# Performance work log

Measured on AMD Instinct MI355X. Metric: run time of the kernel, lower is better.

Reference implementation:

```python
import jax, jax.numpy as jnp
import numpy as np

D = 1024      # embedding_dim
H = 16        # n_heads
HD = D // H   # head_dim = 64
E = 8         # num_experts
K = 2         # top_k
I = 1024      # moe intermediate
S = 2048      # seq_len
B = 1
EPS = 1e-6
THETA = 10000.0


def _rmsnorm(x, w):
    xf = x.astype(jnp.float32)
    var = jnp.mean(xf * xf, axis=-1, keepdims=True)
    return (xf * jax.lax.rsqrt(var + EPS)).astype(x.dtype) * w


def _rope(x, positions):
    # x: [B, S, H, HD], neox-style rotate-half RoPE
    half = HD // 2
    inv_freq = 1.0 / (THETA ** (jnp.arange(0, half, dtype=jnp.float32) / half))
    freqs = positions.astype(jnp.float32)[:, None] * inv_freq[None, :]  # [S, half]
    cos = jnp.cos(freqs)[None, :, None, :]
    sin = jnp.sin(freqs)[None, :, None, :]
    x1, x2 = x[..., :half], x[..., half:]
    return jnp.concatenate([x1 * cos - x2 * sin, x1 * sin + x2 * cos], axis=-1).astype(x.dtype)


def _attn(x, positions, wqkv, wo):
    b, s, _ = x.shape
    qkv = (x @ wqkv).reshape(b, s, 3, H, HD)
    q, k, v = qkv[:, :, 0], qkv[:, :, 1], qkv[:, :, 2]
    q = _rope(q, positions)
    k = _rope(k, positions)
    scale = 1.0 / np.sqrt(HD)
    scores = jnp.einsum('bqhd,bkhd->bhqk', q, k) * scale
    causal = jnp.tril(jnp.ones((s, s), dtype=bool))
    scores = jnp.where(causal[None, None], scores, jnp.finfo(scores.dtype).min)
    probs = jax.nn.softmax(scores, axis=-1)
    o = jnp.einsum('bhqk,bkhd->bqhd', probs, v).reshape(b, s, D)
    return o @ wo


def _moe(x, gate_w, wg, wu, wd):
    # x: [T, D]
    T = x.shape[0]
    logits = x @ gate_w                                    # [T, E]
    probs = jax.nn.softmax(logits.astype(jnp.float32), axis=-1)
    vals, idx = jax.lax.top_k(probs, K)                    # [T, K]
    vals = vals / jnp.sum(vals, axis=-1, keepdims=True)    # renormalize=True
    combine = jnp.zeros((T, E), dtype=jnp.float32)
    combine = combine.at[jnp.arange(T)[:, None], idx].add(vals)
    combine = combine.astype(x.dtype)                      # [T, E]
    out = jnp.zeros_like(x)
    for e in range(E):  # fixed small expert loop; SwiGLU expert FFN
        h = jax.nn.silu(x @ wg[e]) * (x @ wu[e])
        out = out + combine[:, e:e + 1] * (h @ wd[e])
    return out


def setup_inputs() -> dict:
    key = jax.random.key(0)
    ks = jax.random.split(key, 8)
    std = 0.02
    return {
        'positions': jnp.arange(S, dtype=jnp.int32),
        'hidden_states': jax.random.normal(ks[0], (B, S, D), jnp.float32),
        'residual': jax.random.normal(ks[1], (B, S, D), jnp.float32),
        'ln1_w': jnp.ones((D,), jnp.float32),
        'ln2_w': jnp.ones((D,), jnp.float32),
        'wqkv': jax.random.normal(ks[2], (D, 3 * D), jnp.float32) * std,
        'wo': jax.random.normal(ks[3], (D, D), jnp.float32) * std,
        'gate_w': jax.random.normal(ks[4], (D, E), jnp.float32) * std,
        'wg': jax.random.normal(ks[5], (E, D, I), jnp.float32) * std,
        'wu': jax.random.normal(ks[6], (E, D, I), jnp.float32) * std,
        'wd': jax.random.normal(ks[7], (E, I, D), jnp.float32) * std,
    }


def reference(positions, hidden_states, residual, ln1_w, ln2_w, wqkv, wo, gate_w, wg, wu, wd):
    # _forward_with_post_attn_norm: residual arg is overwritten by hidden_states
    res = hidden_states
    x = _rmsnorm(hidden_states, ln1_w)
    x = res + _attn(x, positions, wqkv, wo)
    res2 = x
    y = _rmsnorm(x, ln2_w)
    b, s, _ = y.shape
    moe_out = _moe(y.reshape(-1, D), gate_w, wg, wu, wd).reshape(b, s, D)
    return res2 + moe_out
```

## Files before the change

kernel.cpp:

```cpp
#include <hip/hip_runtime.h>
#include <math.h>

constexpr int S  = 2048;
constexpr int D  = 1024;
constexpr int NH = 16;
constexpr int NE = 8;
constexpr float EPS   = 1e-6f;
constexpr float THETA = 10000.0f;
constexpr float SCL2  = 0.125f * 1.4426950408889634f;
constexpr float LOG2E = 1.4426950408889634f;

typedef unsigned short u16;
typedef unsigned int   u32;
typedef unsigned long long u64;
typedef __attribute__((ext_vector_type(8))) short short8;
typedef __attribute__((ext_vector_type(4))) float f32x4;

__device__ __forceinline__ u16 f2bf(float x) {
  union { float f; u32 u; } v; v.f = x;
  u32 r = (v.u + 0x7FFFu + ((v.u >> 16) & 1u)) >> 16;
  return (u16)r;
}
__device__ __forceinline__ float bf2f(u16 h) {
  union { u32 u; float f; } v; v.u = ((u32)h) << 16;
  return v.f;
}
__device__ __forceinline__ f32x4 mfma16(short8 a, short8 b, f32x4 c) {
  return __builtin_amdgcn_mfma_f32_16x16x32_bf16(a, b, c, 0, 0, 0);
}
__device__ __forceinline__ void gl_lds16(const void* g, void* l) {
  __builtin_amdgcn_global_load_lds((const __attribute__((address_space(1))) u32*)g,
                                   (__attribute__((address_space(3))) u32*)l, 16, 0, 0);
}
__device__ __forceinline__ u64 pack4bf(float a, float b, float c, float d) {
  return (u64)f2bf(a) | ((u64)f2bf(b) << 16) | ((u64)f2bf(c) << 32) | ((u64)f2bf(d) << 48);
}

__global__ __launch_bounds__(256) void prep_kernel(const float* __restrict__ wqkv,
    const float* __restrict__ wo, const float* __restrict__ wg, const float* __restrict__ wu,
    const float* __restrict__ wd, const int* __restrict__ positions,
    const float* __restrict__ hidden, const float* __restrict__ ln1_w,
    u16* __restrict__ wqkvT2, u16* __restrict__ woT2, u16* __restrict__ wgT,
    u16* __restrict__ wuT, u16* __restrict__ wdT, float2* __restrict__ ropetab,
    u16* __restrict__ xn2) {
  const int b = blockIdx.x;
  const int tid = threadIdx.x;
  if (b >= 7424) {
    const int t = b - 7424;
    const float* xr = hidden + (size_t)t * D;
    float v[4]; float ss = 0.f;
#pragma unroll
    for (int i = 0; i < 4; ++i) { v[i] = xr[tid + i * 256]; ss += v[i] * v[i]; }
#pragma unroll
    for (int m = 32; m >= 1; m >>= 1) ss += __shfl_xor(ss, m, 64);
    __shared__ float red[4];
    if ((tid & 63) == 0) red[tid >> 6] = ss;
    __syncthreads();
    const float rs = rsqrtf((red[0] + red[1] + red[2] + red[3]) * (1.f / (float)D) + EPS);
#pragma unroll
    for (int i = 0; i < 4; ++i) {
      const int d = tid + i * 256;
      const float y = v[i] * rs * ln1_w[d];
      const u16 h = f2bf(y);
      xn2[(size_t)t * 2048 + d] = h;
      xn2[(size_t)t * 2048 + 1024 + d] = f2bf(y - bf2f(h));
    }
    return;
  }
  if (b >= 7168) {
    const int idx = (b - 7168) * 256 + tid;
    const int t = idx >> 5, p = idx & 31;
    const float inv = powf(THETA, -(float)p * (1.f / 32.f));
    const float fr = (float)positions[t] * inv;
    float sn, cs; sincosf(fr, &sn, &cs);
    ropetab[idx] = make_float2(cs, sn);
    return;
  }
  __shared__ float t_[64][65];
  const float* W; u16* out; int N, n0, k0; bool split;
  if (b < 768) {
    W = wqkv; out = wqkvT2; N = 3072; split = true;
    n0 = (b % 48) * 64; k0 = (b / 48) * 64;
  } else if (b < 1024) {
    W = wo; out = woT2; N = 1024; split = true;
    const int r = b - 768; n0 = (r & 15) * 64; k0 = (r >> 4) * 64;
  } else {
    int r;
    if (b < 3072)      { r = b - 1024; const int e = r >> 8; W = wg + (size_t)e * 1048576; out = wgT + (size_t)e * 1048576; }
    else if (b < 5120) { r = b - 3072; const int e = r >> 8; W = wu + (size_t)e * 1048576; out = wuT + (size_t)e * 1048576; }
    else               { r = b - 5120; const int e = r >> 8; W = wd + (size_t)e * 1048576; out = wdT + (size_t)e * 1048576; }
    N = 1024; split = false;
    r &= 255; n0 = (r & 15) * 64; k0 = (r >> 4) * 64;
  }
  const int rr = tid >> 4, c4 = (tid & 15) * 4;
#pragma unroll
  for (int i = 0; i < 4; ++i) {
    const float4 v = *(const float4*)(W + (size_t)(k0 + rr + i * 16) * N + n0 + c4);
    t_[rr + i * 16][c4 + 0] = v.x; t_[rr + i * 16][c4 + 1] = v.y;
    t_[rr + i * 16][c4 + 2] = v.z; t_[rr + i * 16][c4 + 3] = v.w;
  }
  __syncthreads();
  if (split) {
#pragma unroll
    for (int i = 0; i < 4; ++i) {
      const int n = n0 + rr + i * 16;
      u16* oh = out + (size_t)n * 2048 + k0 + c4;
      const float v0 = t_[c4 + 0][rr + i * 16], v1 = t_[c4 + 1][rr + i * 16];
      const float v2 = t_[c4 + 2][rr + i * 16], v3 = t_[c4 + 3][rr + i * 16];
      *(u64*)(void*)oh = pack4bf(v0, v1, v2, v3);
      *(u64*)(void*)(oh + 1024) = pack4bf(v0 - bf2f(f2bf(v0)), v1 - bf2f(f2bf(v1)),
                                          v2 - bf2f(f2bf(v2)), v3 - bf2f(f2bf(v3)));
    }
  } else {
#pragma unroll
    for (int i = 0; i < 4; ++i) {
      const int n = n0 + rr + i * 16;
      u16* o = out + (size_t)n * 1024 + k0 + c4;
      *(u64*)(void*)o = pack4bf(t_[c4 + 0][rr + i * 16], t_[c4 + 1][rr + i * 16],
                                t_[c4 + 2][rr + i * 16], t_[c4 + 3][rr + i * 16]);
    }
  }
}

__global__ __launch_bounds__(256) void gemm_qkv(const u16* __restrict__ A2,
    const u16* __restrict__ Bt2, float* __restrict__ Cpart) {
  __shared__ u16 As[2][128 * 32];
  __shared__ u16 Bs[2][128 * 32];
  const int b = blockIdx.x;
  const int xcd = b & 7, ii = b >> 3;
  const int m0 = (ii & 15) * 128;
  const int np = (ii >> 4) % 3, ks = (ii >> 4) / 3;
  const int n0 = (xcd * 3 + np) * 128;
  const int kk0 = ks * 48, kk1 = kk0 + 48;
  const int tid = threadIdx.x, wv = tid >> 6, lane = tid & 63;
  const int l15 = lane & 15, lg = lane >> 4;
  const int wr = wv >> 1, wc = wv & 1;
  const int sr = lane >> 2, sk = (lane & 3) * 16;
  const u16* aptr[2]; const u16* bptr[2];
#pragma unroll
  for (int i = 0; i < 2; ++i) {
    aptr[i] = A2 + (size_t)(m0 + (wv * 2 + i) * 16 + sr) * 2048;
    bptr[i] = Bt2 + (size_t)(n0 + (wv * 2 + i) * 16 + sr) * 2048;
  }
  auto STAGE = [&](int buf, int kk) {
    const int t = kk * 32;
    int ka, kb;
    if (t < 1024)      { ka = t;        kb = t; }
    else if (t < 2048) { ka = t;        kb = t - 1024; }
    else               { ka = t - 2048; kb = t - 1024; }
#pragma unroll
    for (int i = 0; i < 2; ++i) {
      gl_lds16((const char*)(aptr[i] + ka) + sk, (char*)As + buf * 8192 + (wv * 2 + i) * 1024);
      gl_lds16((const char*)(bptr[i] + kb) + sk, (char*)Bs + buf * 8192 + (wv * 2 + i) * 1024);
    }
  };
  f32x4 acc[4][4] = {};
  STAGE(0, kk0);
  __syncthreads();
  int cur = 0;
  for (int kk = kk0; kk < kk1; ++kk) {
    if (kk + 1 < kk1) STAGE(cur ^ 1, kk + 1);
    const u16* Ab = (const u16*)As + cur * 4096;
    const u16* Bb = (const u16*)Bs + cur * 4096;
    short8 a[4], bb[4];
#pragma unroll
    for (int i = 0; i < 4; ++i)
      a[i] = *(const short8*)(const void*)(Ab + (size_t)(wr * 64 + i * 16 + l15) * 32 + lg * 8);
#pragma unroll
    for (int j = 0; j < 4; ++j)
      bb[j] = *(const short8*)(const void*)(Bb + (size_t)(wc * 64 + j * 16 + l15) * 32 + lg * 8);
    __builtin_amdgcn_s_setprio(1);
#pragma unroll
    for (int i = 0; i < 4; ++i)
#pragma unroll
      for (int j = 0; j < 4; ++j) acc[i][j] = mfma16(a[i], bb[j], acc[i][j]);
    __builtin_amdgcn_s_setprio(0);
    __syncthreads();
    cur ^= 1;
  }
  float* P = Cpart + (size_t)ks * S * 3072;
#pragma unroll
  for (int i = 0; i < 4; ++i)
#pragma unroll
    for (int j = 0; j < 4; ++j)
#pragma unroll
      for (int r = 0; r < 4; ++r) {
        const int row = m0 + wr * 64 + i * 16 + lg * 4 + r;
        const int col = n0 + wc * 64 + j * 16 + l15;
        P[(size_t)row * 3072 + col] = acc[i][j][r];
      }
}

__global__ __launch_bounds__(256) void qkv_combine(const float* __restrict__ Cp,
    const float2* __restrict__ tab, u16* __restrict__ Ch, u16* __restrict__ Cl) {
  const int t = blockIdx.x, tid = threadIdx.x;
  const float* r0 = Cp + (size_t)t * 3072;
  const float* r1 = r0 + (size_t)S * 3072;
  const size_t ob = (size_t)t * 3072;
#pragma unroll
  for (int i = 0; i < 4; ++i) {
    const int pi = tid + i * 256;
    const int h = pi >> 5, p = pi & 31;
    const int col = h * 64 + p;
    const float x1 = r0[col] + r1[col];
    const float x2 = r0[col + 32] + r1[col + 32];
    const float2 cs = tab[t * 32 + p];
    const float y1 = x1 * cs.x - x2 * cs.y;
    const float y2 = x1 * cs.y + x2 * cs.x;
    const u16 h1 = f2bf(y1);
    Ch[ob + col] = h1; Cl[ob + col] = f2bf(y1 - bf2f(h1));
    const u16 h2 = f2bf(y2);
    Ch[ob + col + 32] = h2; Cl[ob + col + 32] = f2bf(y2 - bf2f(h2));
  }
#pragma unroll
  for (int i = 0; i < 4; ++i) {
    const int col = 2048 + tid + i * 256;
    const float y = r0[col] + r1[col];
    const u16 h = f2bf(y);
    Ch[ob + col] = h; Cl[ob + col] = f2bf(y - bf2f(h));
  }
}

__global__ __launch_bounds__(256) void gemm_wo(const u16* __restrict__ A2,
    const u16* __restrict__ Bt2, float* __restrict__ Pout) {
  constexpr int N = 1024;
  __shared__ u16 As[2][128 * 32];
  __shared__ u16 Bs[2][128 * 32];
  const int b = blockIdx.x;
  const int xcd = b & 7, ii = b >> 3;
  const int n0 = xcd * 128;
  const int m0 = (ii & 15) * 128;
  const int ks = ii >> 4;
  const int kk0 = ks * 24, kk1 = kk0 + 24;
  const int tid = threadIdx.x, wv = tid >> 6, lane = tid & 63;
  const int l15 = lane & 15, lg = lane >> 4;
  const int wr = wv >> 1, wc = wv & 1;
  const int sr = lane >> 2, sk = (lane & 3) * 16;
  const u16* aptr[2]; const u16* bptr[2];
#pragma unroll
  for (int i = 0; i < 2; ++i) {
    aptr[i] = A2 + (size_t)(m0 + (wv * 2 + i) * 16 + sr) * 2048;
    bptr[i] = Bt2 + (size_t)(n0 + (wv * 2 + i) * 16 + sr) * 2048;
  }
  auto STAGE = [&](int buf, int kk) {
    const int t = kk * 32;
    int ka, kb;
    if (t < 1024)      { ka = t;        kb = t; }
    else if (t < 2048) { ka = t;        kb = t - 1024; }
    else               { ka = t - 2048; kb = t - 1024; }
#pragma unroll
    for (int i = 0; i < 2; ++i) {
      gl_lds16((const char*)(aptr[i] + ka) + sk, (char*)As + buf * 8192 + (wv * 2 + i) * 1024);
      gl_lds16((const char*)(bptr[i] + kb) + sk, (char*)Bs + buf * 8192 + (wv * 2 + i) * 1024);
    }
  };
  f32x4 acc[4][4] = {};
  STAGE(0, kk0);
  __syncthreads();
  int cur = 0;
  for (int kk = kk0; kk < kk1; ++kk) {
    if (kk + 1 < kk1) STAGE(cur ^ 1, kk + 1);
    const u16* Ab = (const u16*)As + cur * 4096;
    const u16* Bb = (const u16*)Bs + cur * 4096;
    short8 a[4], bb[4];
#pragma unroll
    for (int i = 0; i < 4; ++i)
      a[i] = *(const short8*)(const void*)(Ab + (size_t)(wr * 64 + i * 16 + l15) * 32 + lg * 8);
#pragma unroll
    for (int j = 0; j < 4; ++j)
      bb[j] = *(const short8*)(const void*)(Bb + (size_t)(wc * 64 + j * 16 + l15) * 32 + lg * 8);
    __builtin_amdgcn_s_setprio(1);
#pragma unroll
    for (int i = 0; i < 4; ++i)
#pragma unroll
      for (int j = 0; j < 4; ++j) acc[i][j] = mfma16(a[i], bb[j], acc[i][j]);
    __builtin_amdgcn_s_setprio(0);
    __syncthreads();
    cur ^= 1;
  }
  float* P = Pout + (size_t)ks * S * N;
#pragma unroll
  for (int i = 0; i < 4; ++i)
#pragma unroll
    for (int j = 0; j < 4; ++j)
#pragma unroll
      for (int r = 0; r < 4; ++r) {
        const int row = m0 + wr * 64 + i * 16 + lg * 4 + r;
        const int col = n0 + wc * 64 + j * 16 + l15;
        P[(size_t)row * N + col] = acc[i][j][r];
      }
}

__global__ __launch_bounds__(256, 3) void attn_mfma(const u16* __restrict__ Qh,
    const u16* __restrict__ Ql, float* __restrict__ Opart, float2* __restrict__ ml) {
  const int b = blockIdx.x;
  const int head = (b & 7) + 8 * ((b >> 3) & 1);
  const int qb = 31 - ((b >> 4) & 31);
  const int sp = (b >> 9) & 3;
  const int q0 = qb * 64;
  const int ktiles = qb + 1;
  const int kbase = ktiles >> 2, krem = ktiles & 3;
  const int t0 = sp * kbase + (sp < krem ? sp : krem);
  const int t1 = t0 + kbase + (sp < krem ? 1 : 0);
  const int tid = threadIdx.x, w = tid >> 6, lane = tid & 63;
  const int l15 = lane & 15, lg = lane >> 4;
  __shared__ u16 Kh[64 * 64];
  __shared__ u16 Kl[64 * 64];
  __shared__ __align__(16) u16 Vth[64 * 72];
  __shared__ __align__(16) u16 Vtl[64 * 72];
  __shared__ __align__(16) u16 Pp[4][16 * 72];

  short8 qh[2], qlo[2];
  {
    const size_t qbase = (size_t)(q0 + w * 16 + l15) * 3072 + head * 64;
    qh[0]  = *(const short8*)(const void*)(Qh + qbase + lg * 8);
    qh[1]  = *(const short8*)(const void*)(Qh + qbase + 32 + lg * 8);
    qlo[0] = *(const short8*)(const void*)(Ql + qbase + lg * 8);
    qlo[1] = *(const short8*)(const void*)(Ql + qbase + 32 + lg * 8);
  }
  f32x4 oacc[4] = {};
  float m_run = -__builtin_inff(), l_run = 0.f;
  const int qrow0 = q0 + w * 16 + lg * 4;
  const int qcol  = q0 + w * 16 + l15;

  const int vhl = tid >> 7, rem = tid & 127;
  const int vkq = rem & 15, vdg = rem >> 4;
  const u16* vbase = (vhl ? Ql : Qh) + 2048 + head * 64 + vdg * 8;
  u16* vdst = vhl ? Vtl : Vth;
  short8 vr[4];

  auto STAGEK = [&](int kt) {
#pragma unroll
    for (int i = 0; i < 2; ++i) {
      const int inst = w * 2 + i;
      const int key = inst * 8 + (lane >> 3);
      const int db = ((lane & 7) * 16) ^ ((key & 7) << 4);
      gl_lds16((const char*)(Qh + (size_t)(kt * 64 + key) * 3072 + 1024 + head * 64) + db,
               (char*)Kh + inst * 1024);
      gl_lds16((const char*)(Ql + (size_t)(kt * 64 + key) * 3072 + 1024 + head * 64) + db,
               (char*)Kl + inst * 1024);
    }
  };
  auto VLOAD = [&](int kt) {
    const u16* vs = vbase + (size_t)(kt * 64 + vkq * 4) * 3072;
    vr[0] = *(const short8*)(const void*)vs;
    vr[1] = *(const short8*)(const void*)(vs + 3072);
    vr[2] = *(const short8*)(const void*)(vs + 6144);
    vr[3] = *(const short8*)(const void*)(vs + 9216);
  };
  auto VWRITE = [&]() {
#pragma unroll
    for (int jj = 0; jj < 8; ++jj) {
      const u64 pk = (u64)(u16)vr[0][jj] | ((u64)(u16)vr[1][jj] << 16) |
                     ((u64)(u16)vr[2][jj] << 32) | ((u64)(u16)vr[3][jj] << 48);
      *(u64*)(void*)(vdst + (vdg * 8 + jj) * 72 + vkq * 4) = pk;
    }
  };

  if (t0 < t1) {
    STAGEK(t0);
    VLOAD(t0);
    VWRITE();
    __syncthreads();
  }
  for (int t = t0; t < t1; ++t) {
    const int k0 = t * 64;
    const bool more = (t + 1 < t1);
    f32x4 sacc[4];
    __builtin_amdgcn_s_setprio(1);
#pragma unroll
    for (int nt = 0; nt < 4; ++nt) {
      const int key = nt * 16 + l15;
      const char* kbh = (const char*)Kh + key * 128;
      const char* kbl = (const char*)Kl + key * 128;
      const int sw = (key & 7) << 4;
      const short8 kh0 = *(const short8*)(const void*)(kbh + ((lg * 16) ^ sw));
      const short8 kh1 = *(const short8*)(const void*)(kbh + ((64 + lg * 16) ^ sw));
      const short8 kl0 = *(const short8*)(const void*)(kbl + ((lg * 16) ^ sw));
      const short8 kl1 = *(const short8*)(const void*)(kbl + ((64 + lg * 16) ^ sw));
      f32x4 s = {};
      s = mfma16(kh0, qh[0], s);  s = mfma16(kh1, qh[1], s);
      s = mfma16(kh0, qlo[0], s); s = mfma16(kh1, qlo[1], s);
      s = mfma16(kl0, qh[0], s);  s = mfma16(kl1, qh[1], s);
      sacc[nt] = s;
    }
    __builtin_amdgcn_s_setprio(0);
    __syncthreads();
    if (more) { STAGEK(t + 1); VLOAD(t + 1); }
#pragma unroll
    for (int nt = 0; nt < 4; ++nt)
#pragma unroll
      for (int r = 0; r < 4; ++r) sacc[nt][r] *= SCL2;
    if (t == qb) {
#pragma unroll
      for (int nt = 0; nt < 4; ++nt) {
        const int keyb = k0 + nt * 16 + lg * 4;
#pragma unroll
        for (int r = 0; r < 4; ++r)
          if (keyb + r > qcol) sacc[nt][r] = -__builtin_inff();
      }
    }
    float mx = sacc[0][0];
#pragma unroll
    for (int nt = 0; nt < 4; ++nt)
#pragma unroll
      for (int r = 0; r < 4; ++r) mx = fmaxf(mx, sacc[nt][r]);
    mx = fmaxf(mx, __shfl_xor(mx, 16, 64));
    mx = fmaxf(mx, __shfl_xor(mx, 32, 64));
    const bool grow = mx > m_run + 8.f;
    if (__any(grow)) {
      const float m_new = fmaxf(m_run, mx);
      const float fac = __builtin_amdgcn_exp2f(m_run - m_new);
      m_run = m_new;
      l_run *= fac;
      float facB[4];
#pragma unroll
      for (int r = 0; r < 4; ++r) facB[r] = __shfl(fac, lg * 4 + r, 64);
#pragma unroll
      for (int nd = 0; nd < 4; ++nd)
#pragma unroll
        for (int r = 0; r < 4; ++r) oacc[nd][r] *= facB[r];
    }
    float ls = 0.f;
#pragma unroll
    for (int nt = 0; nt < 4; ++nt)
#pragma unroll
      for (int r = 0; r < 4; ++r) {
        sacc[nt][r] = __builtin_amdgcn_exp2f(sacc[nt][r] - m_run);
        ls += sacc[nt][r];
      }
    ls += __shfl_xor(ls, 16, 64);
    ls += __shfl_xor(ls, 32, 64);
    l_run += ls;
    u16* prow = &Pp[w][l15 * 72];
#pragma unroll
    for (int nt = 0; nt < 4; ++nt) {
      const u64 pk = (u64)(__float_as_uint(sacc[nt][0]) >> 16) |
                     ((u64)(__float_as_uint(sacc[nt][1]) >> 16) << 16) |
                     ((u64)(__float_as_uint(sacc[nt][2]) >> 16) << 32) |
                     ((u64)(__float_as_uint(sacc[nt][3]) >> 16) << 48);
      *(u64*)(void*)(prow + nt * 16 + lg * 4) = pk;
    }
    __builtin_amdgcn_s_setprio(1);
#pragma unroll
    for (int kk2 = 0; kk2 < 2; ++kk2) {
      const short8 pa = *(const short8*)(const void*)((const char*)prow + kk2 * 64 + lg * 16);
#pragma unroll
      for (int nd = 0; nd < 4; ++nd) {
        const short8 vbh = *(const short8*)(const void*)((const char*)Vth + (nd * 16 + l15) * 144 + kk2 * 64 + lg * 16);
        const short8 vbl = *(const short8*)(const void*)((const char*)Vtl + (nd * 16 + l15) * 144 + kk2 * 64 + lg * 16);
        oacc[nd] = mfma16(pa, vbh, oacc[nd]);
        oacc[nd] = mfma16(pa, vbl, oacc[nd]);
      }
    }
    __builtin_amdgcn_s_setprio(0);
    asm volatile("" ::: "memory");
#pragma unroll
    for (int nt = 0; nt < 4; ++nt) {
      float lo[4];
#pragma unroll
      for (int r = 0; r < 4; ++r)
        lo[r] = sacc[nt][r] - __uint_as_float(__float_as_uint(sacc[nt][r]) & 0xFFFF0000u);
      const u64 pk = (u64)(__float_as_uint(lo[0]) >> 16) |
                     ((u64)(__float_as_uint(lo[1]) >> 16) << 16) |
                     ((u64)(__float_as_uint(lo[2]) >> 16) << 32) |
                     ((u64)(__float_as_uint(lo[3]) >> 16) << 48);
      *(u64*)(void*)(prow + nt * 16 + lg * 4) = pk;
    }
    asm volatile("" ::: "memory");
    __builtin_amdgcn_s_setprio(1);
#pragma unroll
    for (int kk2 = 0; kk2 < 2; ++kk2) {
      const short8 pa = *(const short8*)(const void*)((const char*)prow + kk2 * 64 + lg * 16);
#pragma unroll
      for (int nd = 0; nd < 4; ++nd) {
        const short8 vbh = *(const short8*)(const void*)((const char*)Vth + (nd * 16 + l15) * 144 + kk2 * 64 + lg * 16);
        oacc[nd] = mfma16(pa, vbh, oacc[nd]);
      }
    }
    __builtin_amdgcn_s_setprio(0);
    __syncthreads();
    if (more) VWRITE();
  }
  float* Op = Opart + (size_t)sp * S * 1024;
#pragma unroll
  for (int nd = 0; nd < 4; ++nd)
#pragma unroll
    for (int r = 0; r < 4; ++r)
      Op[(size_t)(qrow0 + r) * 1024 + head * 64 + nd * 16 + l15] = oacc[nd][r];
  if (lg == 0) {
    ml[((size_t)sp * S + q0 + w * 16 + l15) * NH + head] = make_float2(m_run, l_run);
  }
}

__global__ __launch_bounds__(256) void attn_combine(const float* __restrict__ Op,
    const float2* __restrict__ ml, u16* __restrict__ OA2) {
  const int t = blockIdx.x, tid = threadIdx.x;
  const int h = tid >> 4, dq = (tid & 15) * 4;
  float2 a[4];
  float M = -__builtin_inff();
#pragma unroll
  for (int c = 0; c < 4; ++c) {
    a[c] = ml[((size_t)c * S + t) * NH + h];
    if (a[c].y > 0.f) M = fmaxf(M, a[c].x);
  }
  float e[4], denom = 0.f;
#pragma unroll
  for (int c = 0; c < 4; ++c) {
    e[c] = (a[c].y > 0.f) ? exp2f(a[c].x - M) : 0.f;
    denom += e[c] * a[c].y;
  }
  const float inv = 1.f / denom;
  float ov[4] = {0.f, 0.f, 0.f, 0.f};
#pragma unroll
  for (int c = 0; c < 4; ++c) {
    const float4 v = *(const float4*)(Op + ((size_t)c * S + t) * 1024 + h * 64 + dq);
    ov[0] += e[c] * v.x; ov[1] += e[c] * v.y; ov[2] += e[c] * v.z; ov[3] += e[c] * v.w;
  }
#pragma unroll
  for (int c2 = 0; c2 < 4; ++c2) {
    const float o = ov[c2] * inv;
    const size_t idx = (size_t)t * 2048 + h * 64 + dq + c2;
    const u16 hb = f2bf(o);
    OA2[idx] = hb;
    OA2[idx + 1024] = f2bf(o - bf2f(hb));
  }
}

__global__ __launch_bounds__(256) void rmsnorm_res2_gate(const float* __restrict__ hidden,
    const float* __restrict__ p01, const float* __restrict__ w2, const float* __restrict__ GW,
    float* __restrict__ out, u16* __restrict__ yb,
    int* __restrict__ top2, float2* __restrict__ topw) {
  const int t = blockIdx.x;
  const int d0 = threadIdx.x * 4;
  const size_t base = (size_t)t * D + d0;
  const float4 h4 = *(const float4*)(hidden + base);
  const float4 a4 = *(const float4*)(p01 + base);
  const float4 b4 = *(const float4*)(p01 + (size_t)S * D + base);
  const float4 c4 = *(const float4*)(p01 + 2 * (size_t)S * D + base);
  const float4 e4 = *(const float4*)(p01 + 3 * (size_t)S * D + base);
  float v[4] = {h4.x + a4.x + b4.x + c4.x + e4.x, h4.y + a4.y + b4.y + c4.y + e4.y,
                h4.z + a4.z + b4.z + c4.z + e4.z, h4.w + a4.w + b4.w + c4.w + e4.w};
  float ss = v[0] * v[0] + v[1] * v[1] + v[2] * v[2] + v[3] * v[3];
#pragma unroll
  for (int m = 32; m >= 1; m >>= 1) ss += __shfl_xor(ss, m, 64);
  __shared__ float red[4];
  if ((threadIdx.x & 63) == 0) red[threadIdx.x >> 6] = ss;
  __syncthreads();
  const float rs = rsqrtf((red[0] + red[1] + red[2] + red[3]) * (1.f / (float)D) + EPS);
  const float4 w4 = *(const float4*)(w2 + d0);
  const float y[4] = {v[0] * rs * w4.x, v[1] * rs * w4.y, v[2] * rs * w4.z, v[3] * rs * w4.w};
  *(float4*)(out + base) = make_float4(v[0], v[1], v[2], v[3]);
  *(u64*)(void*)(yb + base) = pack4bf(y[0], y[1], y[2], y[3]);
  float lg[8] = {};
#pragma unroll
  for (int j = 0; j < 4; ++j) {
    const float4 g0 = *(const float4*)(GW + (d0 + j) * 8);
    const float4 g1 = *(const float4*)(GW + (d0 + j) * 8 + 4);
    lg[0] += y[j] * g0.x; lg[1] += y[j] * g0.y; lg[2] += y[j] * g0.z; lg[3] += y[j] * g0.w;
    lg[4] += y[j] * g1.x; lg[5] += y[j] * g1.y; lg[6] += y[j] * g1.z; lg[7] += y[j] * g1.w;
  }
#pragma unroll
  for (int e = 0; e < 8; ++e)
#pragma unroll
    for (int m = 32; m >= 1; m >>= 1) lg[e] += __shfl_xor(lg[e], m, 64);
  __shared__ float wred[4][8];
  if ((threadIdx.x & 63) == 0)
#pragma unroll
    for (int e = 0; e < 8; ++e) wred[threadIdx.x >> 6][e] = lg[e];
  __syncthreads();
  if (threadIdx.x == 0) {
    float L[8];
#pragma unroll
    for (int e = 0; e < 8; ++e) L[e] = wred[0][e] + wred[1][e] + wred[2][e] + wred[3][e];
    int i0 = 0; float v0 = L[0];
    for (int i = 1; i < 8; ++i) if (L[i] > v0) { v0 = L[i]; i0 = i; }
    int i1 = -1; float v1 = -__builtin_inff();
    for (int i = 0; i < 8; ++i) if (i != i0 && L[i] > v1) { v1 = L[i]; i1 = i; }
    const float e1 = expf(v1 - v0);
    const float inv = 1.f / (1.f + e1);
    top2[t] = i0 | (i1 << 4);
    topw[t] = make_float2(inv, e1 * inv);
  }
}

__global__ __launch_bounds__(1024) void scatter_compact(const int* __restrict__ top2,
    const float2* __restrict__ topw, int* __restrict__ counts,
    int* __restrict__ tok_map, float* __restrict__ w_map) {
  const int tid = threadIdx.x;
  __shared__ u64 s0[1024], s1[1024];
  int e_[2][2]; float w_[2][2];
  u64 c0 = 0, c1 = 0;
#pragma unroll
  for (int k = 0; k < 2; ++k) {
    const int t = tid * 2 + k;
    const int pk = top2[t];
    const float2 wv = topw[t];
    e_[k][0] = pk & 15; e_[k][1] = (pk >> 4) & 15;
    w_[k][0] = wv.x;    w_[k][1] = wv.y;
#pragma unroll
    for (int s = 0; s < 2; ++s) {
      const int e = e_[k][s];
      if (e < 4) c0 += 1ull << (e * 16); else c1 += 1ull << ((e - 4) * 16);
    }
  }
  s0[tid] = c0; s1[tid] = c1;
  __syncthreads();
  for (int off = 1; off < 1024; off <<= 1) {
    const u64 a0 = (tid >= off) ? s0[tid - off] : 0;
    const u64 a1 = (tid >= off) ? s1[tid - off] : 0;
    __syncthreads();
    s0[tid] += a0; s1[tid] += a1;
    __syncthreads();
  }
  if (tid == 1023) {
#pragma unroll
    for (int e = 0; e < 4; ++e) counts[e] = (int)((s0[1023] >> (e * 16)) & 0xFFFF);
#pragma unroll
    for (int e = 4; e < 8; ++e) counts[e] = (int)((s1[1023] >> ((e - 4) * 16)) & 0xFFFF);
  }
  u64 l0 = s0[tid] - c0, l1 = s1[tid] - c1;
#pragma unroll
  for (int k = 0; k < 2; ++k) {
    const int t = tid * 2 + k;
#pragma unroll
    for (int s = 0; s < 2; ++s) {
      const int e = e_[k][s];
      int p;
      if (e < 4) { p = (int)((l0 >> (e * 16)) & 0xFFFF); l0 += 1ull << (e * 16); }
      else       { p = (int)((l1 >> ((e - 4) * 16)) & 0xFFFF); l1 += 1ull << ((e - 4) * 16); }
      tok_map[e * S + p] = t | (s << 16);
      w_map[e * S + p] = w_[k][s];
    }
  }
}

__global__ __launch_bounds__(256) void moe_gu(const u16* __restrict__ Yb,
    const u16* __restrict__ Wgb, const u16* __restrict__ Wub, u16* __restrict__ Hb,
    const int* __restrict__ counts, const int* __restrict__ tokmap) {
  const int b = blockIdx.x;
  const int e = b & 7, ii = b >> 3;
  const int n0 = (ii & 15) * 64;
  const int m0 = (ii >> 4) * 128;
  const int cnt = counts[e];
  if (m0 >= cnt) return;
  __shared__ u16 SH[2][16 * 512];
  const int tid = threadIdx.x, wv = tid >> 6, lane = tid & 63;
  const int l15 = lane & 15, lg = lane >> 4;
  const int wr = wv >> 1, wc = wv & 1;
  const int sr = lane >> 2, sk = (lane & 3) * 16;
  const u16* B1 = Wgb + (size_t)e * 1048576;
  const u16* B2 = Wub + (size_t)e * 1048576;
  const u16* cp[4];
#pragma unroll
  for (int i = 0; i < 4; ++i) {
    const int c = wv * 4 + i;
    if (c < 8) {
      const int arow = m0 + c * 16 + sr;
      const int tok = tokmap[e * S + arow] & 2047;
      cp[i] = Yb + (size_t)tok * 1024;
    } else if (c < 12) {
      cp[i] = B1 + (size_t)(n0 + (c - 8) * 16 + sr) * 1024;
    } else {
      cp[i] = B2 + (size_t)(n0 + (c - 12) * 16 + sr) * 1024;
    }
  }
  auto STAGE = [&](int buf, int k) {
#pragma unroll
    for (int i = 0; i < 4; ++i) {
      const int c = wv * 4 + i;
      gl_lds16((const char*)(cp[i] + k) + sk, (char*)SH + buf * 16384 + c * 1024);
    }
  };
  f32x4 acc1[4][2] = {};
  f32x4 acc2[4][2] = {};
  STAGE(0, 0);
  __syncthreads();
  int cur = 0;
  for (int kk = 0; kk < 32; ++kk) {
    if (kk < 31) STAGE(cur ^ 1, (kk + 1) * 32);
    const u16* Sb = (const u16*)SH + cur * 8192;
    short8 a[4], b1f[2], b2f[2];
#pragma unroll
    for (int i = 0; i < 4; ++i)
      a[i] = *(const short8*)(const void*)(Sb + (size_t)(wr * 64 + i * 16 + l15) * 32 + lg * 8);
#pragma unroll
    for (int j = 0; j < 2; ++j) {
      b1f[j] = *(const short8*)(const void*)(Sb + 4096 + (size_t)(wc * 32 + j * 16 + l15) * 32 + lg * 8);
      b2f[j] = *(const short8*)(const void*)(Sb + 6144 + (size_t)(wc * 32 + j * 16 + l15) * 32 + lg * 8);
    }
    __builtin_amdgcn_s_setprio(1);
#pragma unroll
    for (int i = 0; i < 4; ++i)
#pragma unroll
      for (int j = 0; j < 2; ++j) {
        acc1[i][j] = mfma16(a[i], b1f[j], acc1[i][j]);
        acc2[i][j] = mfma16(a[i], b2f[j], acc2[i][j]);
      }
    __builtin_amdgcn_s_setprio(0);
    __syncthreads();
    cur ^= 1;
  }
#pragma unroll
  for (int i = 0; i < 4; ++i)
#pragma unroll
    for (int j = 0; j < 2; ++j)
#pragma unroll
      for (int r = 0; r < 4; ++r) {
        const int row = m0 + wr * 64 + i * 16 + lg * 4 + r;
        if (row < cnt) {
          const float g = acc1[i][j][r];
          const float u = acc2[i][j][r];
          const float sig = __builtin_amdgcn_rcpf(1.f + __builtin_amdgcn_exp2f(-g * LOG2E));
          Hb[((size_t)e * 2048 + row) * 1024 + n0 + wc * 32 + j * 16 + l15] = f2bf(u * g * sig);
        }
      }
}

__global__ __launch_bounds__(256) void moe_down(const u16* __restrict__ Hb,
    const u16* __restrict__ Wdb, u16* __restrict__ slotp,
    const int* __restrict__ counts, const int* __restrict__ tokmap,
    const float* __restrict__ wmap) {
  const int b = blockIdx.x;
  const int e = b & 7, ii = b >> 3;
  const int m0 = (ii & 15) * 128;
  const int n0 = ((ii >> 4) & 7) * 128;
  const int ks = ii >> 7;
  const int cnt = counts[e];
  if (m0 >= cnt) return;
  __shared__ u16 As[2][128 * 32];
  __shared__ u16 Bs[2][128 * 32];
  const int tid = threadIdx.x, wv = tid >> 6, lane = tid & 63;
  const int l15 = lane & 15, lg = lane >> 4;
  const int wr = wv >> 1, wc = wv & 1;
  const int sr = lane >> 2, sk = (lane & 3) * 16;
  const u16* B = Wdb + (size_t)e * 1048576;
  const u16* aptr[2]; const u16* bptr[2];
#pragma unroll
  for (int i = 0; i < 2; ++i) {
    aptr[i] = Hb + ((size_t)e * 2048 + m0 + (wv * 2 + i) * 16 + sr) * 1024;
    bptr[i] = B + (size_t)(n0 + (wv * 2 + i) * 16 + sr) * 1024;
  }
  auto STAGE = [&](int buf, int k) {
#pragma unroll
    for (int i = 0; i < 2; ++i) {
      gl_lds16((const char*)(aptr[i] + k) + sk, (char*)As + buf * 8192 + (wv * 2 + i) * 1024);
      gl_lds16((const char*)(bptr[i] + k) + sk, (char*)Bs + buf * 8192 + (wv * 2 + i) * 1024);
    }
  };
  f32x4 acc[4][4] = {};
  const int kb0 = ks * 16, kb1 = kb0 + 16;
  STAGE(0, kb0 * 32);
  __syncthreads();
  int cur = 0;
  for (int kk = kb0; kk < kb1; ++kk) {
    if (kk + 1 < kb1) STAGE(cur ^ 1, (kk + 1) * 32);
    const u16* Ab = (const u16*)As + cur * 4096;
    const u16* Bb = (const u16*)Bs + cur * 4096;
    short8 a[4], bb[4];
#pragma unroll
    for (int i = 0; i < 4; ++i)
      a[i] = *(const short8*)(const void*)(Ab + (size_t)(wr * 64 + i * 16 + l15) * 32 + lg * 8);
#pragma unroll
    for (int j = 0; j < 4; ++j)
      bb[j] = *(const short8*)(const void*)(Bb + (size_t)(wc * 64 + j * 16 + l15) * 32 + lg * 8);
    __builtin_amdgcn_s_setprio(1);
#pragma unroll
    for (int i = 0; i < 4; ++i)
#pragma unroll
      for (int j = 0; j < 4; ++j) acc[i][j] = mfma16(a[i], bb[j], acc[i][j]);
    __builtin_amdgcn_s_setprio(0);
    __syncthreads();
    cur ^= 1;
  }
#pragma unroll
  for (int i = 0; i < 4; ++i)
#pragma unroll
    for (int j = 0; j < 4; ++j)
#pragma unroll
      for (int r = 0; r < 4; ++r) {
        const int row = m0 + wr * 64 + i * 16 + lg * 4 + r;
        if (row < cnt) {
          const int raw = tokmap[e * S + row];
          const int t = raw & 2047;
          const int sl = (raw >> 16) & 1;
          const float wgt = wmap[e * S + row];
          slotp[((size_t)(sl * 2 + ks) * S + t) * 1024 + n0 + wc * 64 + j * 16 + l15] =
              f2bf(wgt * acc[i][j][r]);
        }
      }
}

__global__ __launch_bounds__(256) void final_add(float* __restrict__ out,
    const u16* __restrict__ sp) {
  const size_t i = ((size_t)blockIdx.x * 256 + threadIdx.x) * 4;
  float4 o = *(float4*)(out + i);
#pragma unroll
  for (int c = 0; c < 4; ++c) {
    const u64 a = *(const u64*)(sp + (size_t)c * S * D + i);
    o.x += bf2f((u16)(a));
    o.y += bf2f((u16)(a >> 16));
    o.z += bf2f((u16)(a >> 32));
    o.w += bf2f((u16)(a >> 48));
  }
  *(float4*)(out + i) = o;
}

extern "C" void kernel_launch(void* const* d_in, const int* in_sizes, int n_in,
                              void* d_out, int out_size, void* d_ws, size_t ws_size,
                              hipStream_t stream) {
  const int*   positions = (const int*)d_in[0];
  const float* hidden    = (const float*)d_in[1];
  const float* ln1_w  = (const float*)d_in[3];
  const float* ln2_w  = (const float*)d_in[4];
  const float* wqkv   = (const float*)d_in[5];
  const float* wo     = (const float*)d_in[6];
  const float* gate_w = (const float*)d_in[7];
  const float* wg     = (const float*)d_in[8];
  const float* wu     = (const float*)d_in[9];
  const float* wd     = (const float*)d_in[10];
  float* out = (float*)d_out;

  char* ws = (char*)d_ws;
  const size_t MB = 1ull << 20;
  u16* wqkvT2 = (u16*)(ws);
  u16* QKVh   = (u16*)(ws);
  u16* OA2    = (u16*)(ws);
  u16* woT2   = (u16*)(ws + 12 * MB);
  u16* wgT    = (u16*)(ws + 16 * MB);
  u16* wuT    = (u16*)(ws + 32 * MB);
  u16* wdT    = (u16*)(ws + 48 * MB);
  float2* ropetab = (float2*)(ws + 64 * MB);
  float2* ml      = (float2*)(ws + 64 * MB + 524288);
  char* mapb = ws + 64 * MB + 1572864;
  int*   counts   = (int*)mapb;
  int*   tok_map  = (int*)(mapb + 512);
  float* w_map    = (float*)(mapb + 512 + 65536);
  int*   top2     = (int*)(mapb + 512 + 131072);
  float2* topw    = (float2*)(mapb + 512 + 139264);
  u16* xn2    = (u16*)(ws + 66 * MB);
  u16* QKVl   = (u16*)(ws + 66 * MB);
  u16* yb     = (u16*)(ws + 66 * MB);
  float* Cpart  = (float*)(ws + 78 * MB);
  float* Opart  = (float*)(ws + 78 * MB);
  float* p01    = (float*)(ws + 78 * MB);
  u16* Hb     = (u16*)(ws + 78 * MB);
  u16* slotp  = (u16*)(ws + 110 * MB);

  prep_kernel<<<9472, 256, 0, stream>>>(wqkv, wo, wg, wu, wd, positions, hidden, ln1_w,
                                        wqkvT2, woT2, wgT, wuT, wdT, ropetab, xn2);
  gemm_qkv<<<768, 256, 0, stream>>>(xn2, wqkvT2, Cpart);
  qkv_combine<<<S, 256, 0, stream>>>(Cpart, ropetab, QKVh, QKVl);
  attn_mfma<<<2048, 256, 0, stream>>>(QKVh, QKVl, Opart, ml);
  attn_combine<<<S, 256, 0, stream>>>(Opart, ml, OA2);
  gemm_wo<<<512, 256, 0, stream>>>(OA2, woT2, p01);
  rmsnorm_res2_gate<<<S, 256, 0, stream>>>(hidden, p01, ln2_w, gate_w, out, yb, top2, topw);
  scatter_compact<<<1, 1024, 0, stream>>>(top2, topw, counts, tok_map, w_map);
  moe_gu<<<2048, 256, 0, stream>>>(yb, wgT, wuT, Hb, counts, tok_map);
  moe_down<<<2048, 256, 0, stream>>>(Hb, wdT, slotp, counts, tok_map, w_map);
  final_add<<<2048, 256, 0, stream>>>(out, slotp);
}
```

Measured before the change: 277.4 us.

## Overlap Wo and MoE weight conversion with attention kernel via extra blocks

Splits the prep kernel so that only the QKV weight transpose, RoPE table and first RMSNorm run before the QKV GEMM. The Wo and expert weight transpose/bf16 conversion blocks are appended to the attention launch, so this memory-bound work can fill CUs left idle by the causal attention's uneven tail. Attention shared memory becomes one union buffer, which may change occupancy slightly. Whether the weight blocks interleave well or contend with attention depends on block dispatch order.

```diff
diff --git a/kernel.cpp b/kernel.cpp
--- a/kernel.cpp
+++ b/kernel.cpp
@@ -36,17 +36,14 @@
   return (u64)f2bf(a) | ((u64)f2bf(b) << 16) | ((u64)f2bf(c) << 32) | ((u64)f2bf(d) << 48);
 }
 
-__global__ __launch_bounds__(256) void prep_kernel(const float* __restrict__ wqkv,
-    const float* __restrict__ wo, const float* __restrict__ wg, const float* __restrict__ wu,
-    const float* __restrict__ wd, const int* __restrict__ positions,
-    const float* __restrict__ hidden, const float* __restrict__ ln1_w,
-    u16* __restrict__ wqkvT2, u16* __restrict__ woT2, u16* __restrict__ wgT,
-    u16* __restrict__ wuT, u16* __restrict__ wdT, float2* __restrict__ ropetab,
-    u16* __restrict__ xn2) {
+__global__ __launch_bounds__(256) void prep_early(const float* __restrict__ wqkv,
+    const int* __restrict__ positions, const float* __restrict__ hidden,
+    const float* __restrict__ ln1_w, u16* __restrict__ wqkvT2,
+    float2* __restrict__ ropetab, u16* __restrict__ xn2) {
   const int b = blockIdx.x;
   const int tid = threadIdx.x;
-  if (b >= 7424) {
-    const int t = b - 7424;
+  if (b >= 1024) {
+    const int t = b - 1024;
     const float* xr = hidden + (size_t)t * D;
     float v[4]; float ss = 0.f;
 #pragma unroll
@@ -67,8 +64,8 @@
     }
     return;
   }
-  if (b >= 7168) {
-    const int idx = (b - 7168) * 256 + tid;
+  if (b >= 768) {
+    const int idx = (b - 768) * 256 + tid;
     const int t = idx >> 5, p = idx & 31;
     const float inv = powf(THETA, -(float)p * (1.f / 32.f));
     const float fr = (float)positions[t] * inv;
@@ -77,48 +74,24 @@
     return;
   }
   __shared__ float t_[64][65];
-  const float* W; u16* out; int N, n0, k0; bool split;
-  if (b < 768) {
-    W = wqkv; out = wqkvT2; N = 3072; split = true;
-    n0 = (b % 48) * 64; k0 = (b / 48) * 64;
-  } else if (b < 1024) {
-    W = wo; out = woT2; N = 1024; split = true;
-    const int r = b - 768; n0 = (r & 15) * 64; k0 = (r >> 4) * 64;
-  } else {
-    int r;
-    if (b < 3072)      { r = b - 1024; const int e = r >> 8; W = wg + (size_t)e * 1048576; out = wgT + (size_t)e * 1048576; }
-    else if (b < 5120) { r = b - 3072; const int e = r >> 8; W = wu + (size_t)e * 1048576; out = wuT + (size_t)e * 1048576; }
-    else               { r = b - 5120; const int e = r >> 8; W = wd + (size_t)e * 1048576; out = wdT + (size_t)e * 1048576; }
-    N = 1024; split = false;
-    r &= 255; n0 = (r & 15) * 64; k0 = (r >> 4) * 64;
-  }
+  const int n0 = (b % 48) * 64, k0 = (b / 48) * 64;
   const int rr = tid >> 4, c4 = (tid & 15) * 4;
 #pragma unroll
   for (int i = 0; i < 4; ++i) {
-    const float4 v = *(const float4*)(W + (size_t)(k0 + rr + i * 16) * N + n0 + c4);
+    const float4 v = *(const float4*)(wqkv + (size_t)(k0 + rr + i * 16) * 3072 + n0 + c4);
     t_[rr + i * 16][c4 + 0] = v.x; t_[rr + i * 16][c4 + 1] = v.y;
     t_[rr + i * 16][c4 + 2] = v.z; t_[rr + i * 16][c4 + 3] = v.w;
   }
   __syncthreads();
-  if (split) {
-#pragma unroll
-    for (int i = 0; i < 4; ++i) {
-      const int n = n0 + rr + i * 16;
-      u16* oh = out + (size_t)n * 2048 + k0 + c4;
-      const float v0 = t_[c4 + 0][rr + i * 16], v1 = t_[c4 + 1][rr + i * 16];
-      const float v2 = t_[c4 + 2][rr + i * 16], v3 = t_[c4 + 3][rr + i * 16];
-      *(u64*)(void*)oh = pack4bf(v0, v1, v2, v3);
-      *(u64*)(void*)(oh + 1024) = pack4bf(v0 - bf2f(f2bf(v0)), v1 - bf2f(f2bf(v1)),
-                                          v2 - bf2f(f2bf(v2)), v3 - bf2f(f2bf(v3)));
-    }
-  } else {
-#pragma unroll
-    for (int i = 0; i < 4; ++i) {
-      const int n = n0 + rr + i * 16;
-      u16* o = out + (size_t)n * 1024 + k0 + c4;
-      *(u64*)(void*)o = pack4bf(t_[c4 + 0][rr + i * 16], t_[c4 + 1][rr + i * 16],
-                                t_[c4 + 2][rr + i * 16], t_[c4 + 3][rr + i * 16]);
-    }
+#pragma unroll
+  for (int i = 0; i < 4; ++i) {
+    const int n = n0 + rr + i * 16;
+    u16* oh = wqkvT2 + (size_t)n * 2048 + k0 + c4;
+    const float v0 = t_[c4 + 0][rr + i * 16], v1 = t_[c4 + 1][rr + i * 16];
+    const float v2 = t_[c4 + 2][rr + i * 16], v3 = t_[c4 + 3][rr + i * 16];
+    *(u64*)(void*)oh = pack4bf(v0, v1, v2, v3);
+    *(u64*)(void*)(oh + 1024) = pack4bf(v0 - bf2f(f2bf(v0)), v1 - bf2f(f2bf(v1)),
+                                        v2 - bf2f(f2bf(v2)), v3 - bf2f(f2bf(v3)));
   }
 }
 
@@ -292,8 +265,69 @@
 }
 
 __global__ __launch_bounds__(256, 3) void attn_mfma(const u16* __restrict__ Qh,
-    const u16* __restrict__ Ql, float* __restrict__ Opart, float2* __restrict__ ml) {
-  const int b = blockIdx.x;
+    const u16* __restrict__ Ql, float* __restrict__ Opart, float2* __restrict__ ml,
+    const float* __restrict__ wo, const float* __restrict__ wg,
+    const float* __restrict__ wu, const float* __restrict__ wd,
+    u16* __restrict__ woT2, u16* __restrict__ wgT, u16* __restrict__ wuT,
+    u16* __restrict__ wdT) {
+  __shared__ __align__(16) char smem[44032];
+  const int bid = blockIdx.x;
+  const int tid = threadIdx.x;
+
+  if (bid >= 2048) {
+    float (*t_)[65] = (float (*)[65])smem;
+    const int b2 = bid - 2048;
+    const float* W; u16* out; bool split;
+    int n0, k0;
+    if (b2 < 256) {
+      W = wo; out = woT2; split = true;
+      n0 = (b2 & 15) * 64; k0 = (b2 >> 4) * 64;
+    } else {
+      int r = b2 - 256;
+      if (r < 2048)       { const int e = r >> 8; W = wg + (size_t)e * 1048576; out = wgT + (size_t)e * 1048576; }
+      else if (r < 4096)  { r -= 2048; const int e = r >> 8; W = wu + (size_t)e * 1048576; out = wuT + (size_t)e * 1048576; }
+      else                { r -= 4096; const int e = r >> 8; W = wd + (size_t)e * 1048576; out = wdT + (size_t)e * 1048576; }
+      split = false;
+      r &= 255; n0 = (r & 15) * 64; k0 = (r >> 4) * 64;
+    }
+    const int rr = tid >> 4, c4 = (tid & 15) * 4;
+#pragma unroll
+    for (int i = 0; i < 4; ++i) {
+      const float4 v = *(const float4*)(W + (size_t)(k0 + rr + i * 16) * 1024 + n0 + c4);
+      t_[rr + i * 16][c4 + 0] = v.x; t_[rr + i * 16][c4 + 1] = v.y;
+      t_[rr + i * 16][c4 + 2] = v.z; t_[rr + i * 16][c4 + 3] = v.w;
+    }
+    __syncthreads();
+    if (split) {
+#pragma unroll
+      for (int i = 0; i < 4; ++i) {
+        const int n = n0 + rr + i * 16;
+        u16* oh = out + (size_t)n * 2048 + k0 + c4;
+        const float v0 = t_[c4 + 0][rr + i * 16], v1 = t_[c4 + 1][rr + i * 16];
+        const float v2 = t_[c4 + 2][rr + i * 16], v3 = t_[c4 + 3][rr + i * 16];
+        *(u64*)(void*)oh = pack4bf(v0, v1, v2, v3);
+        *(u64*)(void*)(oh + 1024) = pack4bf(v0 - bf2f(f2bf(v0)), v1 - bf2f(f2bf(v1)),
+                                            v2 - bf2f(f2bf(v2)), v3 - bf2f(f2bf(v3)));
+      }
+    } else {
+#pragma unroll
+      for (int i = 0; i < 4; ++i) {
+        const int n = n0 + rr + i * 16;
+        *(u64*)(void*)(out + (size_t)n * 1024 + k0 + c4) =
+            pack4bf(t_[c4 + 0][rr + i * 16], t_[c4 + 1][rr + i * 16],
+                    t_[c4 + 2][rr + i * 16], t_[c4 + 3][rr + i * 16]);
+      }
+    }
+    return;
+  }
+
+  u16* Kh  = (u16*)(smem);
+  u16* Kl  = (u16*)(smem + 8192);
+  u16* Vth = (u16*)(smem + 16384);
+  u16* Vtl = (u16*)(smem + 25600);
+  u16* Pp  = (u16*)(smem + 34816);
+
+  const int b = bid;
   const int head = (b & 7) + 8 * ((b >> 3) & 1);
   const int qb = 31 - ((b >> 4) & 31);
   const int sp = (b >> 9) & 3;
@@ -302,13 +336,8 @@
   const int kbase = ktiles >> 2, krem = ktiles & 3;
   const int t0 = sp * kbase + (sp < krem ? sp : krem);
   const int t1 = t0 + kbase + (sp < krem ? 1 : 0);
-  const int tid = threadIdx.x, w = tid >> 6, lane = tid & 63;
+  const int w = tid >> 6, lane = tid & 63;
   const int l15 = lane & 15, lg = lane >> 4;
-  __shared__ u16 Kh[64 * 64];
-  __shared__ u16 Kl[64 * 64];
-  __shared__ __align__(16) u16 Vth[64 * 72];
-  __shared__ __align__(16) u16 Vtl[64 * 72];
-  __shared__ __align__(16) u16 Pp[4][16 * 72];
 
   short8 qh[2], qlo[2];
   {
@@ -432,7 +461,7 @@
     ls += __shfl_xor(ls, 16, 64);
     ls += __shfl_xor(ls, 32, 64);
     l_run += ls;
-    u16* prow = &Pp[w][l15 * 72];
+    u16* prow = Pp + w * 1152 + l15 * 72;
 #pragma unroll
     for (int nt = 0; nt < 4; ++nt) {
       const u64 pk = (u64)(__float_as_uint(sacc[nt][0]) >> 16) |
@@ -847,11 +876,12 @@
   u16* Hb     = (u16*)(ws + 78 * MB);
   u16* slotp  = (u16*)(ws + 110 * MB);
 
-  prep_kernel<<<9472, 256, 0, stream>>>(wqkv, wo, wg, wu, wd, positions, hidden, ln1_w,
-                                        wqkvT2, woT2, wgT, wuT, wdT, ropetab, xn2);
+  prep_early<<<3072, 256, 0, stream>>>(wqkv, positions, hidden, ln1_w,
+                                       wqkvT2, ropetab, xn2);
   gemm_qkv<<<768, 256, 0, stream>>>(xn2, wqkvT2, Cpart);
   qkv_combine<<<S, 256, 0, stream>>>(Cpart, ropetab, QKVh, QKVl);
-  attn_mfma<<<2048, 256, 0, stream>>>(QKVh, QKVl, Opart, ml);
+  attn_mfma<<<8448, 256, 0, stream>>>(QKVh, QKVl, Opart, ml,
+                                      wo, wg, wu, wd, woT2, wgT, wuT, wdT);
   attn_combine<<<S, 256, 0, stream>>>(Opart, ml, OA2);
   gemm_wo<<<512, 256, 0, stream>>>(OA2, woT2, p01);
   rmsnorm_res2_gate<<<S, 256, 0, stream>>>(hidden, p01, ln2_w, gate_w, out, yb, top2, topw);
```

Result: faster. 268.3 us (-3.3%).
